# Optimization experiments

Measured on AMD Instinct MI355X. Metric: run time of the kernel, lower is better.

## Reference

```python
import jax, jax.numpy as jnp
import numpy as np

D_MODEL = 1024
NUM_HEADS = 16
HEAD_DIM = D_MODEL // NUM_HEADS
BATCH = 2
SEQ = 2048


def setup_inputs() -> dict:
    key = jax.random.key(0)
    ks = jax.random.split(key, 12)
    s = 1.0 / np.sqrt(D_MODEL)
    inp = {
        "pre_query": jax.random.normal(ks[0], (BATCH, SEQ, D_MODEL), jnp.float32),
        "pre_key": jax.random.normal(ks[1], (BATCH, SEQ, D_MODEL), jnp.float32),
        "pre_value": jax.random.normal(ks[2], (BATCH, SEQ, D_MODEL), jnp.float32),
        "mask": jnp.ones((SEQ, SEQ), dtype=bool),
        "Wq": jax.random.normal(ks[3], (D_MODEL, D_MODEL), jnp.float32) * s,
        "bq": jax.random.normal(ks[4], (D_MODEL,), jnp.float32) * s,
        "Wk": jax.random.normal(ks[5], (D_MODEL, D_MODEL), jnp.float32) * s,
        "bk": jax.random.normal(ks[6], (D_MODEL,), jnp.float32) * s,
        "Wv": jax.random.normal(ks[7], (D_MODEL, D_MODEL), jnp.float32) * s,
        "bv": jax.random.normal(ks[8], (D_MODEL,), jnp.float32) * s,
        "Wo": jax.random.normal(ks[9], (D_MODEL, D_MODEL), jnp.float32) * s,
        "bo": jax.random.normal(ks[10], (D_MODEL,), jnp.float32) * s,
    }
    return inp


def reference(pre_query, pre_key, pre_value, mask, Wq, bq, Wk, bk, Wv, bv, Wo, bo):
    b = pre_query.shape[0]
    # linear projections (torch Linear: x @ W.T + b); dropout is identity (eval)
    q = (pre_query @ Wq.T + bq).reshape(b, -1, NUM_HEADS, HEAD_DIM)
    k = (pre_key @ Wk.T + bk).reshape(b, -1, NUM_HEADS, HEAD_DIM)
    v = (pre_value @ Wv.T + bv).reshape(b, -1, NUM_HEADS, HEAD_DIM)
    scores = jnp.einsum('blhd,bLhd->bhlL', q, k) / jnp.sqrt(jnp.float32(HEAD_DIM))
    scores = jnp.where(mask, scores, jnp.float32(-jnp.inf))
    attn = jax.nn.softmax(scores, axis=-1)
    out = jnp.einsum('bhlL,bLhd->blhd', attn, v).reshape(b, -1, D_MODEL)
    return out @ Wo.T + bo
```

## Files before the change

### kernel.cpp

```cpp
#include <hip/hip_runtime.h>
#include <hip/hip_bf16.h>

#define DM 1024
#define NH 16
#define HD 64
#define BATCH 2
#define SEQL 2048
#define MROWS (BATCH*SEQL)

typedef unsigned short u16;
typedef __bf16 bf16x8 __attribute__((ext_vector_type(8)));
typedef float f32x4 __attribute__((ext_vector_type(4)));
typedef float f32x16 __attribute__((ext_vector_type(16)));
typedef unsigned u32x4 __attribute__((ext_vector_type(4)));

__device__ __forceinline__ u16 f2bf(float f) {
  __hip_bfloat16 h = __float2bfloat16(f);
  u16 u; __builtin_memcpy(&u, &h, 2); return u;
}

__device__ __forceinline__ unsigned cvt_pk_bf16(float a, float b) {
  unsigned r;
  asm("v_cvt_pk_bf16_f32 %0, %1, %2" : "=v"(r) : "v"(a), "v"(b));
  return r;
}

__device__ __forceinline__ void gload_lds16(const u16* g, u16* l) {
  __builtin_amdgcn_global_load_lds((const __attribute__((address_space(1))) void*)g,
                                   (__attribute__((address_space(3))) void*)l,
                                   16, 0, 0);
}

__global__ __launch_bounds__(256) void cvt_all(const float* __restrict__ s0,
                                               const float* __restrict__ s1,
                                               const float* __restrict__ s2,
                                               const float* __restrict__ s3,
                                               const float* __restrict__ s4,
                                               const float* __restrict__ s5,
                                               const float* __restrict__ s6,
                                               u16* __restrict__ d0,
                                               u16* __restrict__ d1,
                                               u16* __restrict__ d2,
                                               u16* __restrict__ d3,
                                               u16* __restrict__ d4,
                                               u16* __restrict__ d5,
                                               u16* __restrict__ d6) {
  const int NX4 = MROWS * DM / 4;
  const int NW4 = DM * DM / 4;
  const int TOT = 3 * NX4 + 4 * NW4;
  int i = blockIdx.x * blockDim.x + threadIdx.x;
  const int stride = gridDim.x * blockDim.x;
  for (; i < TOT; i += stride) {
    const float* s; u16* d; int j;
    if (i < 3 * NX4) {
      const int a = i >> 20; j = i & (NX4 - 1);
      s = (a == 0) ? s0 : (a == 1) ? s1 : s2;
      d = (a == 0) ? d0 : (a == 1) ? d1 : d2;
    } else {
      const int k = i - 3 * NX4;
      const int a = k >> 18; j = k & (NW4 - 1);
      s = (a == 0) ? s3 : (a == 1) ? s4 : (a == 2) ? s5 : s6;
      d = (a == 0) ? d3 : (a == 1) ? d4 : (a == 2) ? d5 : d6;
    }
    const float4 v = ((const float4*)s)[j];
    ushort4 o;
    o.x = f2bf(v.x); o.y = f2bf(v.y); o.z = f2bf(v.z); o.w = f2bf(v.w);
    ((ushort4*)d)[j] = o;
  }
}

template<int SWAP>
__device__ __forceinline__ void gemm_body(const u16* __restrict__ A,
                                          const u16* __restrict__ W,
                                          u16* As, u16* Bs,
                                          int m0, int n0, f32x4 acc[4][4]) {
  constexpr int KD = DM;
  const int tid = threadIdx.x;
  const int lane = tid & 63, wave = tid >> 6;
  const int wr = wave >> 1, wc = wave & 1;
  const int l15 = lane & 15, g = lane >> 4;
  const int srow = tid >> 2;
  const int scol = (tid & 3) * 8;
  const u16* Ag = A + (size_t)(m0 + srow) * KD + scol;
  const u16* Wg = W + (size_t)(n0 + srow) * KD + scol;

  gload_lds16(Ag,           As + tid * 8);
  gload_lds16(Ag + 64 * KD, As + 2048 + tid * 8);
  gload_lds16(Wg,           Bs + tid * 8);
  gload_lds16(Wg + 64 * KD, Bs + 2048 + tid * 8);

  for (int k0 = 0; k0 < KD; k0 += 32) {
    const int cur = (k0 >> 5) & 1;
    __syncthreads();
    if (k0 + 32 < KD) {
      const int nb = (cur ^ 1) * 4096;
      gload_lds16(Ag + k0 + 32,           As + nb + tid * 8);
      gload_lds16(Ag + k0 + 32 + 64 * KD, As + nb + 2048 + tid * 8);
      gload_lds16(Wg + k0 + 32,           Bs + nb + tid * 8);
      gload_lds16(Wg + k0 + 32 + 64 * KD, Bs + nb + 2048 + tid * 8);
    }
    const u16* Ab = As + cur * 4096;
    const u16* Bb = Bs + cur * 4096;
    bf16x8 a[4], b[4];
#pragma unroll
    for (int mi = 0; mi < 4; ++mi)
      a[mi] = *(const bf16x8*)&Ab[(wr * 64 + mi * 16 + l15) * 32 + g * 8];
#pragma unroll
    for (int ni = 0; ni < 4; ++ni)
      b[ni] = *(const bf16x8*)&Bb[(wc * 64 + ni * 16 + l15) * 32 + g * 8];
#pragma unroll
    for (int mi = 0; mi < 4; ++mi)
#pragma unroll
      for (int ni = 0; ni < 4; ++ni) {
        if (SWAP)
          acc[ni][mi] = __builtin_amdgcn_mfma_f32_16x16x32_bf16(b[ni], a[mi], acc[ni][mi], 0, 0, 0);
        else
          acc[mi][ni] = __builtin_amdgcn_mfma_f32_16x16x32_bf16(a[mi], b[ni], acc[mi][ni], 0, 0, 0);
      }
  }
}

__global__ __launch_bounds__(256) void gemm_qkv(const u16* __restrict__ Xq,
                                                const u16* __restrict__ Xk,
                                                const u16* __restrict__ Xv,
                                                const u16* __restrict__ Wq,
                                                const u16* __restrict__ Wk,
                                                const u16* __restrict__ Wv,
                                                const float* __restrict__ bq,
                                                const float* __restrict__ bk,
                                                const float* __restrict__ bv,
                                                u16* __restrict__ Qw,
                                                u16* __restrict__ Kw,
                                                u16* __restrict__ Vw,
                                                float qscale) {
  __shared__ u16 As[2][128 * 32];
  __shared__ u16 Bs[2][128 * 32];
  const int z = blockIdx.z;
  const u16* A = (z == 0) ? Xq : (z == 1) ? Xk : Xv;
  const u16* W = (z == 0) ? Wq : (z == 1) ? Wk : Wv;
  const float* bias = (z == 0) ? bq : (z == 1) ? bk : bv;
  const float scale = (z == 0) ? qscale : 1.0f;
  const int m0 = blockIdx.x * 128, n0 = blockIdx.y * 128;

  const int tid = threadIdx.x;
  const int lane = tid & 63, wave = tid >> 6;
  const int wr = wave >> 1, wc = wave & 1;
  const int l15 = lane & 15, g = lane >> 4;

  if (z < 2) {
    f32x4 acc[4][4] = {};
    gemm_body<1>(A, W, &As[0][0], &Bs[0][0], m0, n0, acc);
    u16* Y = (z == 0) ? Qw : Kw;
#pragma unroll
    for (int mi = 0; mi < 4; ++mi) {
      const int m = m0 + wr * 64 + mi * 16 + l15;
      const int b = m >> 11, s = m & 2047;
#pragma unroll
      for (int ni = 0; ni < 4; ++ni) {
        const int nb = n0 + wc * 64 + ni * 16 + g * 4;
        const int h = nb >> 6, d0 = nb & 63;
        const float4 bv4 = *(const float4*)&bias[nb];
        ushort4 o;
        o.x = f2bf((acc[ni][mi][0] + bv4.x) * scale);
        o.y = f2bf((acc[ni][mi][1] + bv4.y) * scale);
        o.z = f2bf((acc[ni][mi][2] + bv4.z) * scale);
        o.w = f2bf((acc[ni][mi][3] + bv4.w) * scale);
        *(ushort4*)&Y[((size_t)(b * NH + h) * SEQL + s) * HD + d0] = o;
      }
    }
  } else {
    f32x4 acc[4][4] = {};
    gemm_body<0>(A, W, &As[0][0], &Bs[0][0], m0, n0, acc);
#pragma unroll
    for (int mi = 0; mi < 4; ++mi) {
      const int mb = m0 + wr * 64 + mi * 16 + g * 4;
      const int b = mb >> 11, s0 = mb & 2047;
#pragma unroll
      for (int ni = 0; ni < 4; ++ni) {
        const int n = n0 + wc * 64 + ni * 16 + l15;
        const float bv_ = bias[n];
        const int h = n >> 6, d = n & 63;
        ushort4 o;
        o.x = f2bf(acc[mi][ni][0] + bv_);
        o.y = f2bf(acc[mi][ni][1] + bv_);
        o.z = f2bf(acc[mi][ni][2] + bv_);
        o.w = f2bf(acc[mi][ni][3] + bv_);
        *(ushort4*)&Vw[((size_t)(b * NH + h) * HD + d) * SEQL + s0] = o;
      }
    }
  }
}

__global__ __launch_bounds__(256) void gemm_out(const u16* __restrict__ A,
                                                const u16* __restrict__ W,
                                                const float* __restrict__ bias,
                                                float* __restrict__ Y) {
  __shared__ u16 As[2][128 * 32];
  __shared__ u16 Bs[2][128 * 32];
  const int m0 = blockIdx.x * 128, n0 = blockIdx.y * 128;
  f32x4 acc[4][4] = {};
  gemm_body<1>(A, W, &As[0][0], &Bs[0][0], m0, n0, acc);

  const int tid = threadIdx.x;
  const int lane = tid & 63, wave = tid >> 6;
  const int wr = wave >> 1, wc = wave & 1;
  const int l15 = lane & 15, g = lane >> 4;
#pragma unroll
  for (int mi = 0; mi < 4; ++mi) {
    const int m = m0 + wr * 64 + mi * 16 + l15;
#pragma unroll
    for (int ni = 0; ni < 4; ++ni) {
      const int nb = n0 + wc * 64 + ni * 16 + g * 4;
      const float4 bv4 = *(const float4*)&bias[nb];
      float4 o;
      o.x = acc[ni][mi][0] + bv4.x;
      o.y = acc[ni][mi][1] + bv4.y;
      o.z = acc[ni][mi][2] + bv4.z;
      o.w = acc[ni][mi][3] + bv4.w;
      *(float4*)&Y[(size_t)m * DM + nb] = o;
    }
  }
}

__device__ __forceinline__ void build_pa_half(const f32x16& s, int base, u32x4& pa) {
  unsigned cA = cvt_pk_bf16(s[base + 0], s[base + 1]);
  unsigned cB = cvt_pk_bf16(s[base + 2], s[base + 3]);
  unsigned cC = cvt_pk_bf16(s[base + 4], s[base + 5]);
  unsigned cD = cvt_pk_bf16(s[base + 6], s[base + 7]);
  asm("v_permlane32_swap_b32 %0, %1" : "+v"(cA), "+v"(cC));
  asm("v_permlane32_swap_b32 %0, %1" : "+v"(cB), "+v"(cD));
  pa.x = cA; pa.y = cB; pa.z = cC; pa.w = cD;
}

__device__ __forceinline__ void exp_sum(f32x16& s0, f32x16& s1, float& l) {
  float r0 = 0.f, r1 = 0.f, r2 = 0.f, r3 = 0.f;
#pragma unroll
  for (int r = 0; r < 16; r += 4) {
    s0[r + 0] = __builtin_amdgcn_exp2f(s0[r + 0]);
    s0[r + 1] = __builtin_amdgcn_exp2f(s0[r + 1]);
    s0[r + 2] = __builtin_amdgcn_exp2f(s0[r + 2]);
    s0[r + 3] = __builtin_amdgcn_exp2f(s0[r + 3]);
    r0 += s0[r + 0]; r1 += s0[r + 1]; r2 += s0[r + 2]; r3 += s0[r + 3];
  }
#pragma unroll
  for (int r = 0; r < 16; r += 4) {
    s1[r + 0] = __builtin_amdgcn_exp2f(s1[r + 0]);
    s1[r + 1] = __builtin_amdgcn_exp2f(s1[r + 1]);
    s1[r + 2] = __builtin_amdgcn_exp2f(s1[r + 2]);
    s1[r + 3] = __builtin_amdgcn_exp2f(s1[r + 3]);
    r0 += s1[r + 0]; r1 += s1[r + 1]; r2 += s1[r + 2]; r3 += s1[r + 3];
  }
  l += (r0 + r1) + (r2 + r3);
}

__global__ __launch_bounds__(128) void attn_kernel(const u16* __restrict__ Q,
                                                   const u16* __restrict__ K,
                                                   const u16* __restrict__ Vt,
                                                   u16* __restrict__ O) {
  __shared__ u16 K_lds[2][2][64 * 64];
  __shared__ u16 V_lds[2][2][64 * 64];

  const int tid = threadIdx.x;
  const int lane = tid & 63, wave = tid >> 6;
  const int l31 = lane & 31, hi = lane >> 5;

  const int lid = blockIdx.x;
  const int w = (lid & 7) * 64 + (lid >> 3);
  const int qt = w & 15, bh = w >> 4;

  const u16* Qb = Q  + (size_t)bh * SEQL * HD;
  const u16* Kb = K  + (size_t)bh * SEQL * HD;
  const u16* Vb = Vt + (size_t)bh * HD * SEQL;
  const int q0 = qt * 128 + wave * 64;
  const int qA = q0 + l31, qB = q0 + 32 + l31;
  const int rswz = (l31 & 7) << 3;

  bf16x8 qfA[4], qfB[4];
#pragma unroll
  for (int kk = 0; kk < 4; ++kk) {
    qfA[kk] = *(const bf16x8*)&Qb[(size_t)qA * HD + kk * 16 + hi * 8];
    qfB[kk] = *(const bf16x8*)&Qb[(size_t)qB * HD + kk * 16 + hi * 8];
  }

  f32x16 oA0 = {}, oA1 = {}, oB0 = {}, oB1 = {};
  float lA = 0.f, lB = 0.f;

  const u16* kp_[4];
  const u16* vp_[4];
#pragma unroll
  for (int it = 0; it < 4; ++it) {
    const int c = it * 128 + tid;
    const int r = c >> 3, sl = (c & 7) ^ (r & 7);
    kp_[it] = Kb + (size_t)r * HD + sl * 8;
    vp_[it] = Vb + (size_t)r * SEQL + sl * 8;
  }

  auto stage_pair = [&](int set, int kvbase) {
#pragma unroll
    for (int tile = 0; tile < 2; ++tile) {
#pragma unroll
      for (int it = 0; it < 4; ++it) {
        const int c = it * 128 + tid;
        gload_lds16(kp_[it] + (size_t)(kvbase + tile * 64) * HD, &K_lds[set][tile][c * 8]);
        gload_lds16(vp_[it] + kvbase + tile * 64,                &V_lds[set][tile][c * 8]);
      }
    }
  };

  stage_pair(0, 0);

  const int NT2 = SEQL / 128;
  for (int tt = 0; tt < NT2; ++tt) {
    const int cur = tt & 1;
    __syncthreads();
    if (tt + 1 < NT2) stage_pair(cur ^ 1, (tt + 1) * 128);

    const int t0 = wave & 1;
#pragma unroll
    for (int ti = 0; ti < 2; ++ti) {
      const int tile = t0 ^ ti;
      const u16* Kt = K_lds[cur][tile];
      const u16* Vtile = V_lds[cur][tile];

      f32x16 sA0 = {}, sA1 = {}, sB0 = {}, sB1 = {};
      __builtin_amdgcn_s_setprio(1);
#pragma unroll
      for (int kk = 0; kk < 4; ++kk) {
        const int col = (kk * 16 + hi * 8) ^ rswz;
        bf16x8 k0 = *(const bf16x8*)&Kt[l31 * 64 + col];
        bf16x8 k1 = *(const bf16x8*)&Kt[(32 + l31) * 64 + col];
        sA0 = __builtin_amdgcn_mfma_f32_32x32x16_bf16(k0, qfA[kk], sA0, 0, 0, 0);
        sA1 = __builtin_amdgcn_mfma_f32_32x32x16_bf16(k1, qfA[kk], sA1, 0, 0, 0);
        sB0 = __builtin_amdgcn_mfma_f32_32x32x16_bf16(k0, qfB[kk], sB0, 0, 0, 0);
        sB1 = __builtin_amdgcn_mfma_f32_32x32x16_bf16(k1, qfB[kk], sB1, 0, 0, 0);
      }
      __builtin_amdgcn_s_setprio(0);

      exp_sum(sA0, sA1, lA);
      exp_sum(sB0, sB1, lB);

      u32x4 paA[4], paB[4];
      build_pa_half(sA0, 0, paA[0]);
      build_pa_half(sA0, 8, paA[1]);
      build_pa_half(sA1, 0, paA[2]);
      build_pa_half(sA1, 8, paA[3]);
      build_pa_half(sB0, 0, paB[0]);
      build_pa_half(sB0, 8, paB[1]);
      build_pa_half(sB1, 0, paB[2]);
      build_pa_half(sB1, 8, paB[3]);

      __builtin_amdgcn_s_setprio(1);
#pragma unroll
      for (int ks = 0; ks < 4; ++ks) {
        const int col = (ks * 16 + hi * 8) ^ rswz;
        bf16x8 v0 = *(const bf16x8*)&Vtile[l31 * 64 + col];
        bf16x8 v1 = *(const bf16x8*)&Vtile[(32 + l31) * 64 + col];
        bf16x8 pbA, pbB;
        __builtin_memcpy(&pbA, &paA[ks], 16);
        __builtin_memcpy(&pbB, &paB[ks], 16);
        oA0 = __builtin_amdgcn_mfma_f32_32x32x16_bf16(v0, pbA, oA0, 0, 0, 0);
        oA1 = __builtin_amdgcn_mfma_f32_32x32x16_bf16(v1, pbA, oA1, 0, 0, 0);
        oB0 = __builtin_amdgcn_mfma_f32_32x32x16_bf16(v0, pbB, oB0, 0, 0, 0);
        oB1 = __builtin_amdgcn_mfma_f32_32x32x16_bf16(v1, pbB, oB1, 0, 0, 0);
      }
      __builtin_amdgcn_s_setprio(0);
    }
  }

  lA += __shfl_xor(lA, 32, 64);
  lB += __shfl_xor(lB, 32, 64);
  const float invA = 1.f / lA, invB = 1.f / lB;
  const int b = bh >> 4, h = bh & 15;
  u16* OrowA = O + (size_t)(b * SEQL + qA) * DM + h * HD;
  u16* OrowB = O + (size_t)(b * SEQL + qB) * DM + h * HD;
#pragma unroll
  for (int db = 0; db < 2; ++db) {
#pragma unroll
    for (int rq = 0; rq < 4; ++rq) {
      {
        const f32x16& o_ = db ? oA1 : oA0;
        ushort4 wv;
        wv.x = f2bf(o_[rq * 4 + 0] * invA);
        wv.y = f2bf(o_[rq * 4 + 1] * invA);
        wv.z = f2bf(o_[rq * 4 + 2] * invA);
        wv.w = f2bf(o_[rq * 4 + 3] * invA);
        *(ushort4*)&OrowA[db * 32 + rq * 8 + hi * 4] = wv;
      }
      {
        const f32x16& o_ = db ? oB1 : oB0;
        ushort4 wv;
        wv.x = f2bf(o_[rq * 4 + 0] * invB);
        wv.y = f2bf(o_[rq * 4 + 1] * invB);
        wv.z = f2bf(o_[rq * 4 + 2] * invB);
        wv.w = f2bf(o_[rq * 4 + 3] * invB);
        *(ushort4*)&OrowB[db * 32 + rq * 8 + hi * 4] = wv;
      }
    }
  }
}

extern "C" void kernel_launch(void* const* d_in, const int* in_sizes, int n_in,
                              void* d_out, int out_size, void* d_ws, size_t ws_size,
                              hipStream_t stream) {
  const float* pre_q = (const float*)d_in[0];
  const float* pre_k = (const float*)d_in[1];
  const float* pre_v = (const float*)d_in[2];
  const float* Wq = (const float*)d_in[4];
  const float* bq = (const float*)d_in[5];
  const float* Wk = (const float*)d_in[6];
  const float* bk = (const float*)d_in[7];
  const float* Wv = (const float*)d_in[8];
  const float* bv = (const float*)d_in[9];
  const float* Wo = (const float*)d_in[10];
  const float* bo = (const float*)d_in[11];

  u16* ws  = (u16*)d_ws;
  u16* Xq  = ws;
  u16* Xk  = Xq + (size_t)MROWS * DM;
  u16* Xv  = Xk + (size_t)MROWS * DM;
  u16* Wqb = Xv + (size_t)MROWS * DM;
  u16* Wkb = Wqb + (size_t)DM * DM;
  u16* Wvb = Wkb + (size_t)DM * DM;
  u16* Wob = Wvb + (size_t)DM * DM;
  u16* Qw  = Wob + (size_t)DM * DM;
  u16* Kw  = Qw + (size_t)MROWS * DM;
  u16* Vw  = Kw + (size_t)MROWS * DM;
  u16* Ow  = Vw + (size_t)MROWS * DM;

  cvt_all<<<dim3(2048), 256, 0, stream>>>(pre_q, pre_k, pre_v, Wq, Wk, Wv, Wo,
                                          Xq, Xk, Xv, Wqb, Wkb, Wvb, Wob);

  const float qscale = 0.125f * 1.4426950408889634f;
  gemm_qkv<<<dim3(32, 8, 3), 256, 0, stream>>>(Xq, Xk, Xv, Wqb, Wkb, Wvb,
                                               bq, bk, bv, Qw, Kw, Vw, qscale);

  attn_kernel<<<dim3(512), 128, 0, stream>>>(Qw, Kw, Vw, Ow);

  gemm_out<<<dim3(32, 8), 256, 0, stream>>>(Ow, Wob, bo, (float*)d_out);
}
```

Measured before the change: 138.8 us.

## Split attention KV range across blocks and merge partials in a combine kernel

Each attention block now runs 4 waves over 256 queries against one half of the KV sequence. Per-query unnormalized fp32 partial outputs and row sums are written to workspace slabs that reuse buffers no longer needed at that point. A new combine kernel adds the two halves, normalizes them, and writes the bf16 output. The aim is more KV-tile reuse per block and a shorter serial KV loop, at the cost of extra fp32 global traffic and one more kernel launch.

```diff
diff --git a/kernel.cpp b/kernel.cpp
--- a/kernel.cpp
+++ b/kernel.cpp
@@ -8,6 +8,10 @@
 #define SEQL 2048
 #define MROWS (BATCH*SEQL)
 
+#define MU ((size_t)1<<20)
+#define SLAB_U16 262144
+#define LPART_U16 (29*MU)
+
 typedef unsigned short u16;
 typedef __bf16 bf16x8 __attribute__((ext_vector_type(8)));
 typedef float f32x4 __attribute__((ext_vector_type(4)));
@@ -29,6 +33,14 @@
   __builtin_amdgcn_global_load_lds((const __attribute__((address_space(1))) void*)g,
                                    (__attribute__((address_space(3))) void*)l,
                                    16, 0, 0);
+}
+
+__device__ __forceinline__ float* slab_ptr(u16* ws, int g) {
+  size_t off;
+  if (g < 48)      off = (size_t)g * SLAB_U16;
+  else if (g < 60) off = 12*MU + (size_t)(g - 48) * SLAB_U16;
+  else             off = 28*MU + (size_t)(g - 60) * SLAB_U16;
+  return (float*)(ws + off);
 }
 
 __global__ __launch_bounds__(256) void cvt_all(const float* __restrict__ s0,
@@ -253,10 +265,10 @@
   l += (r0 + r1) + (r2 + r3);
 }
 
-__global__ __launch_bounds__(128) void attn_kernel(const u16* __restrict__ Q,
+__global__ __launch_bounds__(256) void attn_kernel(const u16* __restrict__ Q,
                                                    const u16* __restrict__ K,
                                                    const u16* __restrict__ Vt,
-                                                   u16* __restrict__ O) {
+                                                   u16* ws) {
   __shared__ u16 K_lds[2][2][64 * 64];
   __shared__ u16 V_lds[2][2][64 * 64];
 
@@ -266,14 +278,15 @@
 
   const int lid = blockIdx.x;
   const int w = (lid & 7) * 64 + (lid >> 3);
-  const int qt = w & 15, bh = w >> 4;
+  const int bh = w >> 4, qt = (w >> 1) & 7, kvh = w & 1;
 
   const u16* Qb = Q  + (size_t)bh * SEQL * HD;
   const u16* Kb = K  + (size_t)bh * SEQL * HD;
   const u16* Vb = Vt + (size_t)bh * HD * SEQL;
-  const int q0 = qt * 128 + wave * 64;
+  const int q0 = qt * 256 + wave * 64;
   const int qA = q0 + l31, qB = q0 + 32 + l31;
   const int rswz = (l31 & 7) << 3;
+  const int kvbase = kvh * 1024;
 
   bf16x8 qfA[4], qfB[4];
 #pragma unroll
@@ -285,31 +298,31 @@
   f32x16 oA0 = {}, oA1 = {}, oB0 = {}, oB1 = {};
   float lA = 0.f, lB = 0.f;
 
-  const u16* kp_[4];
-  const u16* vp_[4];
-#pragma unroll
-  for (int it = 0; it < 4; ++it) {
-    const int c = it * 128 + tid;
+  const u16* kp_[2];
+  const u16* vp_[2];
+#pragma unroll
+  for (int it = 0; it < 2; ++it) {
+    const int c = it * 256 + tid;
     const int r = c >> 3, sl = (c & 7) ^ (r & 7);
-    kp_[it] = Kb + (size_t)r * HD + sl * 8;
-    vp_[it] = Vb + (size_t)r * SEQL + sl * 8;
-  }
-
-  auto stage_pair = [&](int set, int kvbase) {
+    kp_[it] = Kb + (size_t)(kvbase + r) * HD + sl * 8;
+    vp_[it] = Vb + (size_t)r * SEQL + kvbase + sl * 8;
+  }
+
+  auto stage_pair = [&](int set, int kvrel) {
 #pragma unroll
     for (int tile = 0; tile < 2; ++tile) {
 #pragma unroll
-      for (int it = 0; it < 4; ++it) {
-        const int c = it * 128 + tid;
-        gload_lds16(kp_[it] + (size_t)(kvbase + tile * 64) * HD, &K_lds[set][tile][c * 8]);
-        gload_lds16(vp_[it] + kvbase + tile * 64,                &V_lds[set][tile][c * 8]);
+      for (int it = 0; it < 2; ++it) {
+        const int c = it * 256 + tid;
+        gload_lds16(kp_[it] + (size_t)(kvrel + tile * 64) * HD, &K_lds[set][tile][c * 8]);
+        gload_lds16(vp_[it] + kvrel + tile * 64,                &V_lds[set][tile][c * 8]);
       }
     }
   };
 
   stage_pair(0, 0);
 
-  const int NT2 = SEQL / 128;
+  const int NT2 = 1024 / 128;
   for (int tt = 0; tt < NT2; ++tt) {
     const int cur = tt & 1;
     __syncthreads();
@@ -369,34 +382,55 @@
 
   lA += __shfl_xor(lA, 32, 64);
   lB += __shfl_xor(lB, 32, 64);
-  const float invA = 1.f / lA, invB = 1.f / lB;
-  const int b = bh >> 4, h = bh & 15;
-  u16* OrowA = O + (size_t)(b * SEQL + qA) * DM + h * HD;
-  u16* OrowB = O + (size_t)(b * SEQL + qB) * DM + h * HD;
+  float* slab = slab_ptr(ws, kvh * 32 + bh);
+  float* lrow = (float*)(ws + LPART_U16) + kvh * 65536 + bh * 2048;
+  if (hi == 0) { lrow[qA] = lA; lrow[qB] = lB; }
 #pragma unroll
   for (int db = 0; db < 2; ++db) {
 #pragma unroll
     for (int rq = 0; rq < 4; ++rq) {
+      const int doff = db * 32 + rq * 8 + hi * 4;
       {
         const f32x16& o_ = db ? oA1 : oA0;
-        ushort4 wv;
-        wv.x = f2bf(o_[rq * 4 + 0] * invA);
-        wv.y = f2bf(o_[rq * 4 + 1] * invA);
-        wv.z = f2bf(o_[rq * 4 + 2] * invA);
-        wv.w = f2bf(o_[rq * 4 + 3] * invA);
-        *(ushort4*)&OrowA[db * 32 + rq * 8 + hi * 4] = wv;
+        float4 wv;
+        wv.x = o_[rq * 4 + 0]; wv.y = o_[rq * 4 + 1];
+        wv.z = o_[rq * 4 + 2]; wv.w = o_[rq * 4 + 3];
+        *(float4*)&slab[qA * 64 + doff] = wv;
       }
       {
         const f32x16& o_ = db ? oB1 : oB0;
-        ushort4 wv;
-        wv.x = f2bf(o_[rq * 4 + 0] * invB);
-        wv.y = f2bf(o_[rq * 4 + 1] * invB);
-        wv.z = f2bf(o_[rq * 4 + 2] * invB);
-        wv.w = f2bf(o_[rq * 4 + 3] * invB);
-        *(ushort4*)&OrowB[db * 32 + rq * 8 + hi * 4] = wv;
-      }
-    }
-  }
+        float4 wv;
+        wv.x = o_[rq * 4 + 0]; wv.y = o_[rq * 4 + 1];
+        wv.z = o_[rq * 4 + 2]; wv.w = o_[rq * 4 + 3];
+        *(float4*)&slab[qB * 64 + doff] = wv;
+      }
+    }
+  }
+}
+
+__global__ __launch_bounds__(256) void combine_kernel(u16* ws, u16* __restrict__ Ow) {
+  const int i = blockIdx.x * 256 + threadIdx.x;
+  const int m = i >> 7;
+  const int c8 = i & 127;
+  const int h = c8 >> 3, d0 = (c8 & 7) * 8;
+  const int b = m >> 11, s = m & 2047;
+  const int bh = b * NH + h;
+  const float* lbase = (const float*)(ws + LPART_U16);
+  const float li = lbase[bh * 2048 + s] + lbase[65536 + bh * 2048 + s];
+  const float inv = 1.0f / li;
+  const float* p0 = slab_ptr(ws, bh)      + (size_t)s * 64 + d0;
+  const float* p1 = slab_ptr(ws, 32 + bh) + (size_t)s * 64 + d0;
+  float4 a0 = *(const float4*)&p0[0];
+  float4 a1 = *(const float4*)&p0[4];
+  float4 b0 = *(const float4*)&p1[0];
+  float4 b1 = *(const float4*)&p1[4];
+  ushort4 o1, o2;
+  o1.x = f2bf((a0.x + b0.x) * inv); o1.y = f2bf((a0.y + b0.y) * inv);
+  o1.z = f2bf((a0.z + b0.z) * inv); o1.w = f2bf((a0.w + b0.w) * inv);
+  o2.x = f2bf((a1.x + b1.x) * inv); o2.y = f2bf((a1.y + b1.y) * inv);
+  o2.z = f2bf((a1.z + b1.z) * inv); o2.w = f2bf((a1.w + b1.w) * inv);
+  *(ushort4*)&Ow[(size_t)m * DM + c8 * 8]     = o1;
+  *(ushort4*)&Ow[(size_t)m * DM + c8 * 8 + 4] = o2;
 }
 
 extern "C" void kernel_launch(void* const* d_in, const int* in_sizes, int n_in,
@@ -416,16 +450,16 @@
 
   u16* ws  = (u16*)d_ws;
   u16* Xq  = ws;
-  u16* Xk  = Xq + (size_t)MROWS * DM;
-  u16* Xv  = Xk + (size_t)MROWS * DM;
-  u16* Wqb = Xv + (size_t)MROWS * DM;
+  u16* Xk  = Xq + 4 * MU;
+  u16* Xv  = Xk + 4 * MU;
+  u16* Wqb = ws + 12 * MU;
   u16* Wkb = Wqb + (size_t)DM * DM;
   u16* Wvb = Wkb + (size_t)DM * DM;
-  u16* Wob = Wvb + (size_t)DM * DM;
-  u16* Qw  = Wob + (size_t)DM * DM;
-  u16* Kw  = Qw + (size_t)MROWS * DM;
-  u16* Vw  = Kw + (size_t)MROWS * DM;
-  u16* Ow  = Vw + (size_t)MROWS * DM;
+  u16* Wob = ws + 15 * MU;
+  u16* Qw  = ws + 16 * MU;
+  u16* Kw  = Qw + 4 * MU;
+  u16* Vw  = Kw + 4 * MU;
+  u16* Ow  = ws + 16 * MU;
 
   cvt_all<<<dim3(2048), 256, 0, stream>>>(pre_q, pre_k, pre_v, Wq, Wk, Wv, Wo,
                                           Xq, Xk, Xv, Wqb, Wkb, Wvb, Wob);
@@ -434,7 +468,9 @@
   gemm_qkv<<<dim3(32, 8, 3), 256, 0, stream>>>(Xq, Xk, Xv, Wqb, Wkb, Wvb,
                                                bq, bk, bv, Qw, Kw, Vw, qscale);
 
-  attn_kernel<<<dim3(512), 128, 0, stream>>>(Qw, Kw, Vw, Ow);
+  attn_kernel<<<dim3(512), 256, 0, stream>>>(Qw, Kw, Vw, ws);
+
+  combine_kernel<<<dim3(2048), 256, 0, stream>>>(ws, Ow);
 
   gemm_out<<<dim3(32, 8), 256, 0, stream>>>(Ow, Wob, bo, (float*)d_out);
 }
```

Measured after the change: 150.2 us. 1.08x slower.
